# Kernel tuning notes

Hardware: AMD Instinct MI355X
Metric: run time of the kernel (lower is better)

The kernel has to match this reference:

```python
import jax, jax.numpy as jnp
import numpy as np
import math

B, N, NDIM = 8, 8192, 2
WIDTH, HEADS, OUT_C, LATENT_D = 128, 4, 128, 128
N_POINT, N_SAMPLE, RADIUS, PATCH = 128, 8, 0.2, 8
MAX_DEG = 15
POS_DIM = NDIM * (1 + 2 * MAX_DEG)  # 62
SELF_LAYERS = 3


def setup_inputs() -> dict:
    ks = jax.random.split(jax.random.key(0), 16)
    f32 = jnp.float32
    def nrm(k, shape, s=0.02):
        return jax.random.normal(k, shape, dtype=f32) * s
    W = WIDTH
    inp = {
        'points': jax.random.uniform(ks[0], (B, N, NDIM), dtype=f32),
        'pe_w': nrm(ks[1], (POS_DIM, W)), 'pe_b': jnp.zeros((W,), f32),
        'conv1_w': nrm(ks[2], (W, W + NDIM, PATCH, 1)), 'conv1_b': jnp.zeros((W,), f32),
        'conv2_w': nrm(ks[3], (W, W, PATCH, 1)), 'conv2_b': jnp.zeros((W,), f32),
        'output_tokens': jax.random.normal(ks[4], (LATENT_D, W), dtype=f32),
        'ln_pre_s': jnp.ones((W,), f32), 'ln_pre_b': jnp.zeros((W,), f32),
        'c_ln1_s': jnp.ones((W,), f32), 'c_ln1_b': jnp.zeros((W,), f32),
        'c_ln2_s': jnp.ones((W,), f32), 'c_ln2_b': jnp.zeros((W,), f32),
        'c_q_w': nrm(ks[5], (W, W)), 'c_q_b': jnp.zeros((W,), f32),
        'c_kv_w': nrm(ks[6], (W, 2 * W)), 'c_kv_b': jnp.zeros((2 * W,), f32),
        'c_proj_w': nrm(ks[7], (W, W)), 'c_proj_b': jnp.zeros((W,), f32),
        'c_ln3_s': jnp.ones((W,), f32), 'c_ln3_b': jnp.zeros((W,), f32),
        'c_mlp1_w': nrm(ks[8], (W, 4 * W)), 'c_mlp1_b': jnp.zeros((4 * W,), f32),
        'c_mlp2_w': nrm(ks[9], (4 * W, W)), 'c_mlp2_b': jnp.zeros((W,), f32),
        's_ln1_s': jnp.ones((SELF_LAYERS, W), f32), 's_ln1_b': jnp.zeros((SELF_LAYERS, W), f32),
        's_qkv_w': nrm(ks[10], (SELF_LAYERS, W, 3 * W)), 's_qkv_b': jnp.zeros((SELF_LAYERS, 3 * W), f32),
        's_proj_w': nrm(ks[11], (SELF_LAYERS, W, W)), 's_proj_b': jnp.zeros((SELF_LAYERS, W), f32),
        's_ln2_s': jnp.ones((SELF_LAYERS, W), f32), 's_ln2_b': jnp.zeros((SELF_LAYERS, W), f32),
        's_mlp1_w': nrm(ks[12], (SELF_LAYERS, W, 4 * W)), 's_mlp1_b': jnp.zeros((SELF_LAYERS, 4 * W), f32),
        's_mlp2_w': nrm(ks[13], (SELF_LAYERS, 4 * W, W)), 's_mlp2_b': jnp.zeros((SELF_LAYERS, W), f32),
        'ln_post_s': jnp.ones((W,), f32), 'ln_post_b': jnp.zeros((W,), f32),
        'out_w': nrm(ks[14], (W, OUT_C)), 'out_b': jnp.zeros((OUT_C,), f32),
    }
    return inp


def _layer_norm(x, s, b):
    m = jnp.mean(x, -1, keepdims=True)
    v = jnp.mean(jnp.square(x - m), -1, keepdims=True)
    return (x - m) * jax.lax.rsqrt(v + 1e-5) * s + b


def _posenc_nerf(x):
    # point-e nerf posenc: concat([x, sin(xb), sin(xb + pi/2)])
    scales = 2.0 ** jnp.arange(MAX_DEG, dtype=jnp.float32)
    xb = (x[..., None, :] * scales[:, None]).reshape(*x.shape[:-1], -1)
    emb = jnp.sin(jnp.concatenate([xb, xb + 0.5 * jnp.pi], axis=-1))
    return jnp.concatenate([x, emb], axis=-1)  # [..., C*(1+2*MAX_DEG)]


def _mha(q, k, v):
    b, tq, w = q.shape
    dh = w // HEADS
    qh = q.reshape(b, tq, HEADS, dh)
    kh = k.reshape(b, -1, HEADS, dh)
    vh = v.reshape(b, -1, HEADS, dh)
    scores = jnp.einsum('bqhd,bkhd->bhqk', qh, kh) * (1.0 / math.sqrt(dh))
    attn = jax.nn.softmax(scores, axis=-1)
    return jnp.einsum('bhqk,bkhd->bqhd', attn, vh).reshape(b, tq, w)


def _circ_conv(x, w, b):
    # Conv2d kernel (PATCH,1), stride 1, circular padding (PATCH//2, 0)
    p = PATCH // 2
    xp = jnp.concatenate([x[:, :, -p:], x, x[:, :, :p]], axis=2)
    y = jax.lax.conv_general_dilated(xp, w, (1, 1), 'VALID',
                                     dimension_numbers=('NCHW', 'OIHW', 'NCHW'))
    return y + b[None, :, None, None]


def _forward(points, pe_w, pe_b, conv1_w, conv1_b, conv2_w, conv2_b, output_tokens,
             ln_pre_s, ln_pre_b, c_ln1_s, c_ln1_b, c_ln2_s, c_ln2_b, c_q_w, c_q_b,
             c_kv_w, c_kv_b, c_proj_w, c_proj_b, c_ln3_s, c_ln3_b, c_mlp1_w, c_mlp1_b,
             c_mlp2_w, c_mlp2_b, s_ln1_s, s_ln1_b, s_qkv_w, s_qkv_b, s_proj_w, s_proj_b,
             s_ln2_s, s_ln2_b, s_mlp1_w, s_mlp1_b, s_mlp2_w, s_mlp2_b, ln_post_s, ln_post_b,
             out_w, out_b):
    bsz, n, _ = points.shape
    dataset_emb = _posenc_nerf(points) @ pe_w + pe_b             # [B,N,W]
    # ---- PointSetEmbedding (fps_method='first' -> first n_point centers) ----
    new_xyz = points[:, :N_POINT]                                # [B,S,2]
    sqr = jnp.sum(jnp.square(new_xyz[:, :, None] - points[:, None]), -1)  # [B,S,N]
    base = jnp.broadcast_to(jnp.arange(n, dtype=jnp.int32), sqr.shape)
    idx = jnp.where(sqr > RADIUS ** 2, n, base)
    idx = jnp.sort(idx, axis=-1)[:, :, :N_SAMPLE]
    idx = jnp.where(idx == n, idx[:, :, :1], idx)                # [B,S,K] ball-query indices
    gather = jax.vmap(lambda a, i: a[i])
    grouped_xyz = gather(points, idx) - new_xyz[:, :, None]      # [B,S,K,2] relative coords
    grouped_pts = gather(dataset_emb, idx)                       # [B,S,K,W]
    feats = jnp.concatenate([grouped_xyz, grouped_pts], -1)      # [B,S,K,W+2]
    x = jnp.transpose(feats, (0, 3, 2, 1))                       # [B,C,K,S]
    x = jax.nn.silu(_circ_conv(x, conv1_w, conv1_b))
    x = jax.nn.silu(_circ_conv(x, conv2_w, conv2_b))
    data_tokens = jnp.transpose(x.mean(axis=2), (0, 2, 1))       # [B,S,W]
    # ---- Perceiver: cross-attn then self-attn ----
    lat = jnp.broadcast_to(output_tokens[None], (bsz, LATENT_D, WIDTH))
    h = _layer_norm(jnp.concatenate([data_tokens, lat], axis=1), ln_pre_s, ln_pre_b)
    q = _layer_norm(h, c_ln1_s, c_ln1_b) @ c_q_w + c_q_b
    kv = _layer_norm(dataset_emb, c_ln2_s, c_ln2_b) @ c_kv_w + c_kv_b
    k, v = jnp.split(kv, 2, axis=-1)
    h = h + (_mha(q, k, v) @ c_proj_w + c_proj_b)
    t = _layer_norm(h, c_ln3_s, c_ln3_b)
    h = h + (jax.nn.gelu(t @ c_mlp1_w + c_mlp1_b, approximate=False) @ c_mlp2_w + c_mlp2_b)
    for i in range(SELF_LAYERS):
        qkv = _layer_norm(h, s_ln1_s[i], s_ln1_b[i]) @ s_qkv_w[i] + s_qkv_b[i]
        q, k, v = jnp.split(qkv, 3, axis=-1)
        h = h + (_mha(q, k, v) @ s_proj_w[i] + s_proj_b[i])
        t = _layer_norm(h, s_ln2_s[i], s_ln2_b[i])
        h = h + (jax.nn.gelu(t @ s_mlp1_w[i] + s_mlp1_b[i], approximate=False) @ s_mlp2_w[i] + s_mlp2_b[i])
    h = h[:, -LATENT_D:]
    return jnp.tanh(_layer_norm(h, ln_post_s, ln_post_b) @ out_w + out_b)


def reference(points, pe_w, pe_b, conv1_w, conv1_b, conv2_w, conv2_b, output_tokens,
              ln_pre_s, ln_pre_b, c_ln1_s, c_ln1_b, c_ln2_s, c_ln2_b, c_q_w, c_q_b,
              c_kv_w, c_kv_b, c_proj_w, c_proj_b, c_ln3_s, c_ln3_b, c_mlp1_w, c_mlp1_b,
              c_mlp2_w, c_mlp2_b, s_ln1_s, s_ln1_b, s_qkv_w, s_qkv_b, s_proj_w, s_proj_b,
              s_ln2_s, s_ln2_b, s_mlp1_w, s_mlp1_b, s_mlp2_w, s_mlp2_b, ln_post_s, ln_post_b,
              out_w, out_b):
    return _forward(points, pe_w, pe_b, conv1_w, conv1_b, conv2_w, conv2_b, output_tokens,
                    ln_pre_s, ln_pre_b, c_ln1_s, c_ln1_b, c_ln2_s, c_ln2_b, c_q_w, c_q_b,
                    c_kv_w, c_kv_b, c_proj_w, c_proj_b, c_ln3_s, c_ln3_b, c_mlp1_w, c_mlp1_b,
                    c_mlp2_w, c_mlp2_b, s_ln1_s, s_ln1_b, s_qkv_w, s_qkv_b, s_proj_w, s_proj_b,
                    s_ln2_s, s_ln2_b, s_mlp1_w, s_mlp1_b, s_mlp2_w, s_mlp2_b, ln_post_s, ln_post_b,
                    out_w, out_b)
```

## Files before the change

### kernel.cpp

```cpp
#include <hip/hip_runtime.h>
#include <math.h>


namespace {

constexpr int NP = 8192;
constexpr int WD = 128;
constexpr int POSD = 62;
constexpr float R2C = 0.04f;
constexpr float QSCALE = 0.17677669529663687f;
constexpr float HALFPI = 1.5707963705062866f;

typedef __bf16 bf16x8 __attribute__((ext_vector_type(8)));
typedef float f32x4 __attribute__((ext_vector_type(4)));
union U16B { uint4 u; bf16x8 h; unsigned short s[8]; };

__device__ __forceinline__ float b2f(unsigned short u) {
  unsigned v = (unsigned)u << 16;
  return __builtin_bit_cast(float, v);
}

constexpr size_t AO_WQ     = 0;
constexpr size_t AO_WKV    = 16384;
constexpr size_t AO_WPROJC = 49152;
constexpr size_t AO_WMLP1C = 65536;
constexpr size_t AO_WMLP2C = 131072;
constexpr size_t AO_WQKVS  = 196608;
constexpr size_t AO_WPROJS = 344064;
constexpr size_t AO_WMLP1S = 393216;
constexpr size_t AO_WMLP2S = 589824;
constexpr size_t AO_WOUT   = 786432;
constexpr size_t AO_W1B    = 802816;
constexpr size_t AO_W2B    = 937984;
constexpr size_t AO_TOT    = 1069056;

__global__ __launch_bounds__(256) void k_posenc(
    const float* __restrict__ pts, const float* __restrict__ pew,
    const float* __restrict__ peb, unsigned short* __restrict__ embb) {
  __shared__ float posT[62][36];
  const int tid = threadIdx.x;
  const int base = blockIdx.x * 32;
  for (int i = tid; i < 32 * POSD; i += 256) {
    int p = i / POSD, j = i % POSD;
    const float* pp = pts + (size_t)(base + p) * 2;
    float v;
    if (j < 2) {
      v = pp[j];
    } else if (j < 32) {
      int t = j - 2;
      v = sinf(pp[t & 1] * (float)(1 << (t >> 1)));
    } else {
      int t = j - 32;
      v = sinf(pp[t & 1] * (float)(1 << (t >> 1)) + HALFPI);
    }
    posT[j][p] = v;
  }
  __syncthreads();
  const int c = tid & 127, pg = tid >> 7;
  float acc[16];
  const float bias = peb[c];
#pragma unroll
  for (int k = 0; k < 16; ++k) acc[k] = bias;
  for (int j = 0; j < POSD; ++j) {
    float w = pew[j * WD + c];
    const float4 p0 = *(const float4*)&posT[j][pg * 16];
    const float4 p1 = *(const float4*)&posT[j][pg * 16 + 4];
    const float4 p2 = *(const float4*)&posT[j][pg * 16 + 8];
    const float4 p3 = *(const float4*)&posT[j][pg * 16 + 12];
    acc[0] += p0.x * w;  acc[1] += p0.y * w;
    acc[2] += p0.z * w;  acc[3] += p0.w * w;
    acc[4] += p1.x * w;  acc[5] += p1.y * w;
    acc[6] += p1.z * w;  acc[7] += p1.w * w;
    acc[8] += p2.x * w;  acc[9] += p2.y * w;
    acc[10] += p2.z * w; acc[11] += p2.w * w;
    acc[12] += p3.x * w; acc[13] += p3.y * w;
    acc[14] += p3.z * w; acc[15] += p3.w * w;
  }
#pragma unroll
  for (int k = 0; k < 16; ++k) {
    __bf16 bv = (__bf16)acc[k];
    embb[(size_t)(base + pg * 16 + k) * WD + c] = *(unsigned short*)&bv;
  }
}

__global__ __launch_bounds__(256) void k_prep(
    const float* __restrict__ wq, const float* __restrict__ wkv,
    const float* __restrict__ wprojc, const float* __restrict__ wmlp1c,
    const float* __restrict__ wmlp2c, const float* __restrict__ wqkvs,
    const float* __restrict__ wprojs, const float* __restrict__ wmlp1s,
    const float* __restrict__ wmlp2s, const float* __restrict__ wout,
    const float* __restrict__ w1, const float* __restrict__ w2,
    unsigned short* __restrict__ dst) {
  const size_t i = (size_t)blockIdx.x * 256 + threadIdx.x;
  if (i >= AO_TOT) return;
  float v;
  if (i < AO_WKV) {
    size_t j = i;            v = wq[(j & 127) * 128 + (j >> 7)];
  } else if (i < AO_WPROJC) {
    size_t j = i - AO_WKV;   v = wkv[(j & 127) * 256 + (j >> 7)];
  } else if (i < AO_WMLP1C) {
    size_t j = i - AO_WPROJC; v = wprojc[(j & 127) * 128 + (j >> 7)];
  } else if (i < AO_WMLP2C) {
    size_t j = i - AO_WMLP1C; v = wmlp1c[(j & 127) * 512 + (j >> 7)];
  } else if (i < AO_WQKVS) {
    size_t j = i - AO_WMLP2C; v = wmlp2c[(j & 511) * 128 + (j >> 9)];
  } else if (i < AO_WPROJS) {
    size_t j = i - AO_WQKVS;
    size_t L = j / 49152, jj = j % 49152;
    v = wqkvs[L * 49152 + (jj & 127) * 384 + (jj >> 7)];
  } else if (i < AO_WMLP1S) {
    size_t j = i - AO_WPROJS;
    size_t L = j / 16384, jj = j % 16384;
    v = wprojs[L * 16384 + (jj & 127) * 128 + (jj >> 7)];
  } else if (i < AO_WMLP2S) {
    size_t j = i - AO_WMLP1S;
    size_t L = j / 65536, jj = j % 65536;
    v = wmlp1s[L * 65536 + (jj & 127) * 512 + (jj >> 7)];
  } else if (i < AO_WOUT) {
    size_t j = i - AO_WMLP2S;
    size_t L = j / 65536, jj = j % 65536;
    v = wmlp2s[L * 65536 + (jj & 511) * 128 + (jj >> 9)];
  } else if (i < AO_W1B) {
    size_t j = i - AO_WOUT;  v = wout[(j & 127) * 128 + (j >> 7)];
  } else if (i < AO_W2B) {
    size_t j = i - AO_W1B;
    size_t c = j / 1056, k = j % 1056;
    v = (k < 1040) ? w1[c * 1040 + k] : 0.f;
  } else {
    size_t j = i - AO_W2B;   v = w2[(j >> 10) * 1024 + (j & 1023)];
  }
  __bf16 bv = (__bf16)v;
  dst[i] = *(unsigned short*)&bv;
}

__global__ __launch_bounds__(256) void k_kvgc(
    const unsigned short* __restrict__ embb,
    const unsigned short* __restrict__ wkvt,
    const float* __restrict__ kvbias, unsigned short* __restrict__ kb,
    unsigned short* __restrict__ vb, const float* __restrict__ lnS,
    const float* __restrict__ lnB, const float* __restrict__ pts,
    const unsigned short* __restrict__ w1b, const float* __restrict__ b1,
    const unsigned short* __restrict__ w2b, const float* __restrict__ b2,
    float* __restrict__ dtok) {
  __shared__ __align__(16) char shl[43776];
  __shared__ int sid[4][8];
  const int bx = blockIdx.x;
  const int tid = threadIdx.x;
  const int w = tid >> 6, lane = tid & 63;
  const int l15 = lane & 15, l16 = lane >> 4;

  if (bx >= 256) {
    const int kx = bx - 256;
    const size_t row0 = (size_t)kx * 32;
    unsigned short (*Ab)[136] = (unsigned short(*)[136])shl;
    unsigned short (*Bt)[136] = (unsigned short(*)[136])(shl + 8704);
    {
      const int n = tid >> 1, hf = tid & 1;
      const unsigned short* src = wkvt + ((size_t)n * 128 + hf * 64);
#pragma unroll
      for (int q8 = 0; q8 < 8; ++q8)
        *(uint4*)&Bt[n][hf * 64 + q8 * 8] = *(const uint4*)(src + q8 * 8);
    }
    {
      const int r = tid >> 3, seg = tid & 7;
      const unsigned short* ap = embb + (row0 + r) * WD + seg * 16;
      U16B w0, w1u;
      w0.u = *(const uint4*)ap;
      w1u.u = *(const uint4*)(ap + 8);
      float xv[16];
#pragma unroll
      for (int j = 0; j < 8; ++j) {
        xv[j] = b2f(w0.s[j]);
        xv[8 + j] = b2f(w1u.s[j]);
      }
      float s = 0.f, sq = 0.f;
#pragma unroll
      for (int j = 0; j < 16; ++j) { s += xv[j]; sq += xv[j] * xv[j]; }
      s += __shfl_xor(s, 1);  sq += __shfl_xor(sq, 1);
      s += __shfl_xor(s, 2);  sq += __shfl_xor(sq, 2);
      s += __shfl_xor(s, 4);  sq += __shfl_xor(sq, 4);
      const float m = s * (1.f / 128.f);
      const float var = fmaxf(sq * (1.f / 128.f) - m * m, 0.f);
      const float rinv = 1.0f / sqrtf(var + 1e-5f);
      U16B u0, u1;
#pragma unroll
      for (int j = 0; j < 16; ++j) {
        int col = seg * 16 + j;
        float y = (xv[j] - m) * rinv * lnS[col] + lnB[col];
        if (j < 8) u0.h[j] = (__bf16)y; else u1.h[j - 8] = (__bf16)y;
      }
      *(uint4*)&Ab[r][seg * 16] = u0.u;
      *(uint4*)&Ab[r][seg * 16 + 8] = u1.u;
    }
    const int rt = w >> 1, ch = w & 1;
    for (int nb = 0; nb < 2; ++nb) {
      if (nb) {
        __syncthreads();
        const int n = tid >> 1, hf = tid & 1;
        const unsigned short* src =
            wkvt + ((size_t)(128 + n) * 128 + hf * 64);
#pragma unroll
        for (int q8 = 0; q8 < 8; ++q8)
          *(uint4*)&Bt[n][hf * 64 + q8 * 8] = *(const uint4*)(src + q8 * 8);
      }
      __syncthreads();
      f32x4 acc[4];
#pragma unroll
      for (int j = 0; j < 4; ++j) acc[j] = (f32x4){0.f, 0.f, 0.f, 0.f};
#pragma unroll
      for (int kk = 0; kk < 4; ++kk) {
        U16B ua;
        ua.u = *(const uint4*)&Ab[rt * 16 + l15][kk * 32 + l16 * 8];
#pragma unroll
        for (int ct4 = 0; ct4 < 4; ++ct4) {
          U16B ub;
          ub.u =
              *(const uint4*)&Bt[(ch * 4 + ct4) * 16 + l15][kk * 32 + l16 * 8];
          acc[ct4] = __builtin_amdgcn_mfma_f32_16x16x32_bf16(ua.h, ub.h,
                                                             acc[ct4], 0, 0, 0);
        }
      }
      unsigned short* Dp = nb ? vb : kb;
#pragma unroll
      for (int ct4 = 0; ct4 < 4; ++ct4) {
        int colL = (ch * 4 + ct4) * 16 + l15;
        float bv = kvbias[nb * 128 + colL];
#pragma unroll
        for (int r = 0; r < 4; ++r) {
          size_t row = row0 + rt * 16 + l16 * 4 + r;
          __bf16 ov = (__bf16)(acc[ct4][r] + bv);
          Dp[row * 128 + colL] = *(unsigned short*)&ov;
        }
      }
    }
    return;
  }

  const int b = bx >> 5;
  const int i0 = (bx & 31) * 4;
  unsigned short* ftp  = (unsigned short*)shl;
  unsigned short* Bt1p = (unsigned short*)(shl + 8448);
  unsigned short* y1p  = (unsigned short*)shl;
  unsigned short* Bt2p = (unsigned short*)(shl + 16384);
  float* tmpp = (float*)(shl + 16384);

  {
    const int i = i0 + w;
    const float cx = pts[((size_t)b * NP + i) * 2];
    const float cy = pts[((size_t)b * NP + i) * 2 + 1];
    int cnt = 0;
    for (int j0 = 0; j0 < NP; j0 += 64) {
      int j = j0 + lane;
      float dx = pts[((size_t)b * NP + j) * 2] - cx;
      float dy = pts[((size_t)b * NP + j) * 2 + 1] - cy;
      float d2 = __fadd_rn(__fmul_rn(dx, dx), __fmul_rn(dy, dy));
      bool ok = !(d2 > R2C);
      unsigned long long m = __ballot(ok);
      int ord = cnt + __popcll(m & ((1ull << lane) - 1ull));
      if (ok && ord < 8) sid[w][ord] = j;
      cnt += (int)__popcll(m);
      if (cnt >= 8) break;
    }
    if (lane < 8 && lane >= cnt) sid[w][lane] = sid[w][0];
  }
  __syncthreads();
  {
    const int pr = tid >> 3, c16 = tid & 7;
    const int pt = pr >> 3, s = pr & 7;
    const unsigned short* src =
        embb + ((size_t)b * NP + sid[pt][s]) * WD + c16 * 16;
    U16B u0, u1;
    u0.u = *(const uint4*)src;
    u1.u = *(const uint4*)(src + 8);
#pragma unroll
    for (int j = 0; j < 8; ++j) {
      ftp[((size_t)pt * 132 + 2 + c16 * 16 + j) * 8 + s] = u0.s[j];
      ftp[((size_t)pt * 132 + 2 + c16 * 16 + 8 + j) * 8 + s] = u1.s[j];
    }
  }
  if (tid < 64) {
    int pt = tid >> 4, rem = tid & 15;
    int s = rem >> 1, d = rem & 1;
    float dv = pts[((size_t)b * NP + sid[pt][s]) * 2 + d] -
               pts[((size_t)b * NP + i0 + pt) * 2 + d];
    __bf16 bv = (__bf16)dv;
    ftp[((size_t)pt * 132 + d) * 8 + s] = *(unsigned short*)&bv;
    int pt2 = tid >> 4, cin2 = 130 + ((tid >> 3) & 1), s2 = tid & 7;
    ftp[((size_t)pt2 * 132 + cin2) * 8 + s2] = 0;
  }
  __syncthreads();
  f32x4 acc1[2][2];
#pragma unroll
  for (int t = 0; t < 2; ++t)
#pragma unroll
    for (int bt = 0; bt < 2; ++bt) acc1[t][bt] = (f32x4){0.f, 0.f, 0.f, 0.f};
  for (int ps = 0; ps < 2; ++ps) {
    const int cinbase = ps ? 68 : 0;
    const int CW = ps ? 64 : 68;
    if (ps) __syncthreads();
    {
      const int n = tid >> 3, g = tid & 7;
      const int pt = n >> 3, h = n & 7;
#pragma unroll
      for (int it = 0; it < 9; ++it) {
        int cl = g + it * 8;
        if (cl < CW) {
          int cin = cinbase + cl;
          U16B u0, u;
          u0.u = *(const uint4*)&ftp[((size_t)pt * 132 + cin) * 8];
#pragma unroll
          for (int p = 0; p < 8; ++p) u.s[p] = u0.s[(h + p + 4) & 7];
          *(uint4*)&Bt1p[n * 552 + cl * 8] = u.u;
        }
      }
    }
    __syncthreads();
    const unsigned short* w1r =
        w1b + (size_t)(w * 32 + l15) * 1056 + cinbase * 8;
    const int kit = ps ? 16 : 17;
    for (int ks = 0; ks < kit; ++ks) {
      const int k0 = ks * 32 + l16 * 8;
      U16B a0, a1, b0, b1u;
      a0.u = *(const uint4*)(w1r + k0);
      a1.u = *(const uint4*)(w1r + 16 * 1056 + k0);
      b0.u = *(const uint4*)&Bt1p[l15 * 552 + k0];
      b1u.u = *(const uint4*)&Bt1p[(16 + l15) * 552 + k0];
      acc1[0][0] = __builtin_amdgcn_mfma_f32_16x16x32_bf16(a0.h, b0.h,
                                                           acc1[0][0], 0, 0, 0);
      acc1[0][1] = __builtin_amdgcn_mfma_f32_16x16x32_bf16(a0.h, b1u.h,
                                                           acc1[0][1], 0, 0, 0);
      acc1[1][0] = __builtin_amdgcn_mfma_f32_16x16x32_bf16(a1.h, b0.h,
                                                           acc1[1][0], 0, 0, 0);
      acc1[1][1] = __builtin_amdgcn_mfma_f32_16x16x32_bf16(a1.h, b1u.h,
                                                           acc1[1][1], 0, 0, 0);
    }
  }
  __syncthreads();
  {
#pragma unroll
    for (int t = 0; t < 2; ++t)
#pragma unroll
      for (int bt = 0; bt < 2; ++bt) {
        const int n = bt * 16 + l15;
        const int pt = n >> 3, h = n & 7;
#pragma unroll
        for (int r = 0; r < 4; ++r) {
          int c = w * 32 + t * 16 + l16 * 4 + r;
          float x = acc1[t][bt][r] + b1[c];
          float sy = x / (1.f + __expf(-x));
          __bf16 bh = (__bf16)sy;
          unsigned short bits = *(unsigned short*)&bh;
          size_t yb = ((size_t)pt * 128 + c) * 16;
          y1p[yb + h] = bits;
          if (h == 0) y1p[yb + 8] = bits;
        }
      }
  }
  f32x4 acc2[2][3];
#pragma unroll
  for (int t = 0; t < 2; ++t)
#pragma unroll
    for (int bt = 0; bt < 3; ++bt) acc2[t][bt] = (f32x4){0.f, 0.f, 0.f, 0.f};
  for (int ps = 0; ps < 4; ++ps) {
    __syncthreads();
    {
      const int g = tid & 7;
      for (int n2 = tid >> 3; n2 < 38; n2 += 32) {
        const int pt = n2 / 9, h2 = n2 % 9;
#pragma unroll
        for (int it = 0; it < 4; ++it) {
          int cl = g + it * 8;
          U16B o;
          if (n2 < 36) {
            int c1 = ps * 32 + cl;
            size_t yb = ((size_t)pt * 128 + c1) * 16;
            U16B u0;
            u0.u = *(const uint4*)&y1p[yb];
            unsigned short yv[9];
#pragma unroll
            for (int j = 0; j < 8; ++j) yv[j] = u0.s[j];
            yv[8] = y1p[yb + 8];
#pragma unroll
            for (int p = 0; p < 8; ++p) o.s[p] = yv[(h2 + p + 5) % 9];
          } else {
            o.u.x = o.u.y = o.u.z = o.u.w = 0;
          }
          *(uint4*)&Bt2p[n2 * 264 + cl * 8] = o.u;
        }
      }
    }
    __syncthreads();
    const unsigned short* w2r =
        w2b + (size_t)(w * 32 + l15) * 1024 + ps * 256;
    int r2 = 32 + l15;
    if (r2 > 37) r2 = 37;
#pragma unroll
    for (int ks = 0; ks < 8; ++ks) {
      const int k0 = ks * 32 + l16 * 8;
      U16B a0, a1, b0, b1u, b2u;
      a0.u = *(const uint4*)(w2r + k0);
      a1.u = *(const uint4*)(w2r + 16 * 1024 + k0);
      b0.u = *(const uint4*)&Bt2p[l15 * 264 + k0];
      b1u.u = *(const uint4*)&Bt2p[(16 + l15) * 264 + k0];
      b2u.u = *(const uint4*)&Bt2p[r2 * 264 + k0];
      acc2[0][0] = __builtin_amdgcn_mfma_f32_16x16x32_bf16(a0.h, b0.h,
                                                           acc2[0][0], 0, 0, 0);
      acc2[0][1] = __builtin_amdgcn_mfma_f32_16x16x32_bf16(a0.h, b1u.h,
                                                           acc2[0][1], 0, 0, 0);
      acc2[0][2] = __builtin_amdgcn_mfma_f32_16x16x32_bf16(a0.h, b2u.h,
                                                           acc2[0][2], 0, 0, 0);
      acc2[1][0] = __builtin_amdgcn_mfma_f32_16x16x32_bf16(a1.h, b0.h,
                                                           acc2[1][0], 0, 0, 0);
      acc2[1][1] = __builtin_amdgcn_mfma_f32_16x16x32_bf16(a1.h, b1u.h,
                                                           acc2[1][1], 0, 0, 0);
      acc2[1][2] = __builtin_amdgcn_mfma_f32_16x16x32_bf16(a1.h, b2u.h,
                                                           acc2[1][2], 0, 0, 0);
    }
  }
  __syncthreads();
  {
#pragma unroll
    for (int t = 0; t < 2; ++t)
#pragma unroll
      for (int bt = 0; bt < 3; ++bt) {
        const int n2 = bt * 16 + l15;
        if (n2 < 36) {
          const int h2 = n2 % 9;
          const float wgt = (h2 == 0) ? 2.f : 1.f;
#pragma unroll
          for (int r = 0; r < 4; ++r) {
            int c = w * 32 + t * 16 + l16 * 4 + r;
            float x = acc2[t][bt][r] + b2[c];
            tmpp[n2 * 132 + c] = wgt * (x / (1.f + __expf(-x)));
          }
        }
      }
  }
  __syncthreads();
#pragma unroll
  for (int k = 0; k < 2; ++k) {
    int idx = tid + k * 256;
    int pt = idx >> 7, c = idx & 127;
    float ssum = 0.f;
#pragma unroll
    for (int h2 = 0; h2 < 9; ++h2) ssum += tmpp[(pt * 9 + h2) * 132 + c];
    dtok[((size_t)b * 128 + i0 + pt) * WD + c] = ssum / 10.0f;
  }
}

__global__ __launch_bounds__(64) void k_concat_ln(
    const float* __restrict__ dtok, const float* __restrict__ otok,
    const float* __restrict__ g, const float* __restrict__ bta,
    float* __restrict__ h0) {
  const int row = blockIdx.x;
  const int b = row >> 8, t = row & 255;
  const int lane = threadIdx.x;
  const float* src = (t < 128) ? (dtok + ((size_t)b * 128 + t) * WD)
                               : (otok + (size_t)(t - 128) * WD);
  const float2 x2 = *(const float2*)(src + lane * 2);
  float s = x2.x + x2.y;
  float sq = x2.x * x2.x + x2.y * x2.y;
#pragma unroll
  for (int o = 1; o < 64; o <<= 1) {
    s += __shfl_xor(s, o);
    sq += __shfl_xor(sq, o);
  }
  float m = s * (1.f / 128.f);
  float var = fmaxf(sq * (1.f / 128.f) - m * m, 0.f);
  float r = 1.0f / sqrtf(var + 1e-5f);
  int c = lane * 2;
  float2 o2;
  o2.x = (x2.x - m) * r * g[c] + bta[c];
  o2.y = (x2.y - m) * r * g[c + 1] + bta[c + 1];
  *(float2*)(h0 + (size_t)row * WD + c) = o2;
}

template <int ABF, int OBF, int COMB>
__global__ __launch_bounds__(256) void k_bgemm16(
    const void* __restrict__ A, int lda, const unsigned short* __restrict__ wt,
    const float* __restrict__ bias, const float* __restrict__ res, int ldres,
    void* __restrict__ D, int ldd, int K, int act,
    const float* __restrict__ lnS, const float* __restrict__ lnB, int keep,
    int skip, float oscale, int scaleCols,
    const unsigned short* __restrict__ opart, const float* __restrict__ lbuf,
    int S) {
  __shared__ unsigned short Ab[16][136];
  __shared__ unsigned short Bt[64][136];
  const int tid = threadIdx.x;
  const int row0 = blockIdx.x * 16;
  const int col0 = blockIdx.y * 64;
  const int w = tid >> 6, lane = tid & 63;
  const int l15 = lane & 15, l16 = lane >> 4;
  f32x4 acc = (f32x4){0.f, 0.f, 0.f, 0.f};
  for (int kt = 0; kt < K; kt += 128) {
    if (kt) __syncthreads();
    {
      const int n = tid >> 2, q = tid & 3;
      const unsigned short* src = wt + (size_t)(col0 + n) * K + kt + q * 32;
      *(uint4*)&Bt[n][q * 32] = *(const uint4*)src;
      *(uint4*)&Bt[n][q * 32 + 8] = *(const uint4*)(src + 8);
// ... 25 lines not shown
        const int srow = (grow / keep) * (keep + skip) + skip + grow % keep;
        const unsigned short* ap =
            (const unsigned short*)A + (size_t)srow * lda + kt + seg * 8;
        *(uint4*)&Ab[r][seg * 8] = *(const uint4*)ap;
      } else {
        const int srow = (grow / keep) * (keep + skip) + skip + grow % keep;
        const float* ap = (const float*)A + (size_t)srow * lda + kt + seg * 8;
        float4 v0 = *(const float4*)ap;
        float4 v1 = *(const float4*)(ap + 4);
        float xv[8] = {v0.x, v0.y, v0.z, v0.w, v1.x, v1.y, v1.z, v1.w};
        if (lnS != nullptr) {
          float s = 0.f, sq = 0.f;
#pragma unroll
          for (int j = 0; j < 8; ++j) { s += xv[j]; sq += xv[j] * xv[j]; }
          s += __shfl_xor(s, 1);  sq += __shfl_xor(sq, 1);
          s += __shfl_xor(s, 2);  sq += __shfl_xor(sq, 2);
          s += __shfl_xor(s, 4);  sq += __shfl_xor(sq, 4);
          s += __shfl_xor(s, 8);  sq += __shfl_xor(sq, 8);
          const float m = s * (1.f / 128.f);
          const float var = fmaxf(sq * (1.f / 128.f) - m * m, 0.f);
          const float rinv = 1.0f / sqrtf(var + 1e-5f);
#pragma unroll
          for (int j = 0; j < 8; ++j) {
            int col = seg * 8 + j;
            xv[j] = (xv[j] - m) * rinv * lnS[col] + lnB[col];
          }
        }
        U16B u0;
#pragma unroll
        for (int j = 0; j < 8; ++j) u0.h[j] = (__bf16)xv[j];
        *(uint4*)&Ab[r][seg * 8] = u0.u;
      }
    }
    __syncthreads();
#pragma unroll
    for (int kk = 0; kk < 4; ++kk) {
      U16B ua, ub;
      ua.u = *(const uint4*)&Ab[l15][kk * 32 + l16 * 8];
      ub.u = *(const uint4*)&Bt[w * 16 + l15][kk * 32 + l16 * 8];
      acc = __builtin_amdgcn_mfma_f32_16x16x32_bf16(ua.h, ub.h, acc, 0, 0, 0);
    }
  }
  {
    const int colL = w * 16 + l15;
    const int col = col0 + colL;
    const float bv = bias[col];
#pragma unroll
    for (int r = 0; r < 4; ++r) {
      const int row = row0 + l16 * 4 + r;
      float x = acc[r] + bv;
      if (col0 < scaleCols) x *= oscale;
      if (act == 1) x = 0.5f * x * (1.0f + erff(x * 0.7071067811865476f));
      else if (act == 2) x = tanhf(x);
      if (res != nullptr) x += res[(size_t)row * ldres + col];
      if (OBF) {
        __bf16 ov = (__bf16)x;
        ((unsigned short*)D)[(size_t)row * ldd + col] = *(unsigned short*)&ov;
      } else {
        ((float*)D)[(size_t)row * ldd + col] = x;
      }
    }
  }
}

__global__ __launch_bounds__(256) void k_attn_mfma(
    const unsigned short* __restrict__ Q, int qs,
    const unsigned short* __restrict__ K, int ks,
    const unsigned short* __restrict__ V, int vs,
    unsigned short* __restrict__ opart, float* __restrict__ lbuf, int Tk,
    int S, int CH) {
  const int bx = blockIdx.x;
  const int s = bx % S;
  const int bh = bx / S;
  const int h = bh & 3, b = bh >> 2;
  const int tid = threadIdx.x;
  const int w = tid >> 6, lane = tid & 63;
  const int l15 = lane & 15, l16 = lane >> 4;

  __shared__ unsigned short Vt[32 * 68];
  __shared__ unsigned short Pl[4][16 * 72];

  bf16x8 qf[4];
#pragma unroll
  for (int m = 0; m < 4; ++m) {
    U16B u;
    u.u = *(const uint4*)(Q + (size_t)(b * 256 + w * 64 + m * 16 + l15) * qs +
                          h * 32 + l16 * 8);
    qf[m] = u.h;
  }
  U16B uones;
#pragma unroll
  for (int j = 0; j < 8; ++j) uones.h[j] = (__bf16)1.0f;
  const bf16x8 ones = uones.h;

  f32x4 o[4][2];
#pragma unroll
  for (int m = 0; m < 4; ++m)
#pragma unroll
    for (int d = 0; d < 2; ++d) o[m][d] = (f32x4){0.f, 0.f, 0.f, 0.f};
  f32x4 lsum[4];
#pragma unroll
  for (int m = 0; m < 4; ++m) lsum[m] = (f32x4){0.f, 0.f, 0.f, 0.f};

  const int kt0 = s * CH;
  for (int kt = kt0; kt < kt0 + CH; kt += 64) {
    __syncthreads();
// ... 94 lines not shown
  const float* conv1_b  = (const float*)d_in[4];
  const float* conv2_w  = (const float*)d_in[5];
  const float* conv2_b  = (const float*)d_in[6];
  const float* otok     = (const float*)d_in[7];
  const float* ln_pre_s = (const float*)d_in[8];
  const float* ln_pre_b = (const float*)d_in[9];
  const float* c_ln1_s  = (const float*)d_in[10];
  const float* c_ln1_b  = (const float*)d_in[11];
  const float* c_ln2_s  = (const float*)d_in[12];
  const float* c_ln2_b  = (const float*)d_in[13];
  const float* c_q_w    = (const float*)d_in[14];
  const float* c_q_b    = (const float*)d_in[15];
  const float* c_kv_w   = (const float*)d_in[16];
  const float* c_kv_b   = (const float*)d_in[17];
  const float* c_proj_w = (const float*)d_in[18];
  const float* c_proj_b = (const float*)d_in[19];
  const float* c_ln3_s  = (const float*)d_in[20];
  const float* c_ln3_b  = (const float*)d_in[21];
  const float* c_mlp1_w = (const float*)d_in[22];
  const float* c_mlp1_b = (const float*)d_in[23];
  const float* c_mlp2_w = (const float*)d_in[24];
  const float* c_mlp2_b = (const float*)d_in[25];
  const float* s_ln1_s  = (const float*)d_in[26];
  const float* s_ln1_b  = (const float*)d_in[27];
  const float* s_qkv_w  = (const float*)d_in[28];
  const float* s_qkv_b  = (const float*)d_in[29];
  const float* s_proj_w = (const float*)d_in[30];
  const float* s_proj_b = (const float*)d_in[31];
  const float* s_ln2_s  = (const float*)d_in[32];
  const float* s_ln2_b  = (const float*)d_in[33];
  const float* s_mlp1_w = (const float*)d_in[34];
  const float* s_mlp1_b = (const float*)d_in[35];
  const float* s_mlp2_w = (const float*)d_in[36];
  const float* s_mlp2_b = (const float*)d_in[37];
  const float* lnpost_s = (const float*)d_in[38];
  const float* lnpost_b = (const float*)d_in[39];
  const float* out_w    = (const float*)d_in[40];
  const float* out_b    = (const float*)d_in[41];

  char* ws = (char*)d_ws;
  constexpr size_t MB = 1024 * 1024;
  unsigned short* embb = (unsigned short*)(ws);
  unsigned short* kbuf = (unsigned short*)(ws + 32 * MB);
  unsigned short* vbuf = (unsigned short*)(ws + 48 * MB);
  char*  b3   = ws + 64 * MB;
  float* dtok = (float*)(b3);
  float* hbuf = (float*)(b3 + 524288);
  unsigned short* qbuf = (unsigned short*)(b3 + 524288 + 1048576);
  unsigned short* mid = (unsigned short*)(b3 + 524288 + 3145728);
  unsigned short* qkv = (unsigned short*)(b3 + 524288 + 7340032);
  unsigned short* arena = (unsigned short*)(b3 + 524288 + 10485760);
  unsigned short* opart = (unsigned short*)(ws);
  float* lbuf  = (float*)(b3 + 16 * MB);

  const int IDK = 1 << 28;

  k_prep<<<(int)((AO_TOT + 255) / 256), 256, 0, stream>>>(
      c_q_w, c_kv_w, c_proj_w, c_mlp1_w, c_mlp2_w, s_qkv_w, s_proj_w,
      s_mlp1_w, s_mlp2_w, out_w, conv1_w, conv2_w, arena);
  k_posenc<<<2048, 256, 0, stream>>>(pts, pe_w, pe_b, embb);
  k_kvgc<<<2304, 256, 0, stream>>>(embb, arena + AO_WKV, c_kv_b, kbuf, vbuf,
                                   c_ln2_s, c_ln2_b, pts, arena + AO_W1B,
                                   conv1_b, arena + AO_W2B, conv2_b, dtok);
  k_concat_ln<<<2048, 64, 0, stream>>>(dtok, otok, ln_pre_s, ln_pre_b, hbuf);
  k_bgemm16<0, 1, 0><<<dim3(128, 2), 256, 0, stream>>>(
      hbuf, 128, arena + AO_WQ, c_q_b, nullptr, 0, qbuf, 128, 128, 0, c_ln1_s,
      c_ln1_b, IDK, 0, QSCALE, 128, nullptr, nullptr, 0);
  k_attn_mfma<<<1024, 256, 0, stream>>>(qbuf, 128, kbuf, 128, vbuf, 128,
                                        opart, lbuf, 8192, 32, 256);
  k_bgemm16<0, 0, 1><<<dim3(128, 2), 256, 0, stream>>>(
      nullptr, 128, arena + AO_WPROJC, c_proj_b, hbuf, 128, hbuf, 128, 128, 0,
      nullptr, nullptr, IDK, 0, 1.f, 0, opart, lbuf, 32);
  k_bgemm16<0, 1, 0><<<dim3(128, 8), 256, 0, stream>>>(
      hbuf, 128, arena + AO_WMLP1C, c_mlp1_b, nullptr, 0, mid, 512, 128, 1,
      c_ln3_s, c_ln3_b, IDK, 0, 1.f, 0, nullptr, nullptr, 0);
  k_bgemm16<1, 0, 0><<<dim3(128, 2), 256, 0, stream>>>(
      mid, 512, arena + AO_WMLP2C, c_mlp2_b, hbuf, 128, hbuf, 128, 512, 0,
      nullptr, nullptr, IDK, 0, 1.f, 0, nullptr, nullptr, 0);
  for (int i = 0; i < 3; ++i) {
    k_bgemm16<0, 1, 0><<<dim3(128, 6), 256, 0, stream>>>(
        hbuf, 128, arena + AO_WQKVS + (size_t)i * 49152, s_qkv_b + i * 384,
        nullptr, 0, qkv, 384, 128, 0, s_ln1_s + i * 128, s_ln1_b + i * 128,
        IDK, 0, QSCALE, 128, nullptr, nullptr, 0);
    k_attn_mfma<<<128, 256, 0, stream>>>(qkv, 384, qkv + 128, 384, qkv + 256,
                                         384, opart, lbuf, 256, 4, 64);
    k_bgemm16<0, 0, 1><<<dim3(128, 2), 256, 0, stream>>>(
        nullptr, 128, arena + AO_WPROJS + (size_t)i * 16384,
        s_proj_b + i * 128, hbuf, 128, hbuf, 128, 128, 0, nullptr, nullptr,
        IDK, 0, 1.f, 0, opart, lbuf, 4);
    k_bgemm16<0, 1, 0><<<dim3(128, 8), 256, 0, stream>>>(
        hbuf, 128, arena + AO_WMLP1S + (size_t)i * 65536, s_mlp1_b + i * 512,
        nullptr, 0, mid, 512, 128, 1, s_ln2_s + i * 128, s_ln2_b + i * 128,
        IDK, 0, 1.f, 0, nullptr, nullptr, 0);
    k_bgemm16<1, 0, 0><<<dim3(128, 2), 256, 0, stream>>>(
        mid, 512, arena + AO_WMLP2S + (size_t)i * 65536, s_mlp2_b + i * 128,
        hbuf, 128, hbuf, 128, 512, 0, nullptr, nullptr, IDK, 0, 1.f, 0,
        nullptr, nullptr, 0);
  }
  k_bgemm16<0, 0, 0><<<dim3(64, 2), 256, 0, stream>>>(
      hbuf, 128, arena + AO_WOUT, out_b, nullptr, 0, (float*)d_out, 128, 128,
      2, lnpost_s, lnpost_b, 128, 128, 1.f, 0, nullptr, nullptr, 0);
}
```

Baseline: 231.6 us.

## Split fused grouping-conv kernel into im2col plus generic GEMM launches

The monolithic k_kvgc kernel, which did ball-query grouping, two patch convolutions and the KV projection in one launch, is split into separate kernels. The new path is a ball-query/im2col kernel, a generic bgemm with a SiLU epilogue for conv1, a second im2col, a bgemm for conv2, a mean-reduction kernel, and a standalone LN+KV kernel. The aim is better parallelism and occupancy for the conv GEMMs, which previously ran in only 256 blocks with large shared memory. In exchange it adds several launches and global-memory round trips for the im2col buffers and intermediate activations.

```diff
diff --git a/kernel.cpp b/kernel.cpp
--- a/kernel.cpp
+++ b/kernel.cpp
@@ -31,8 +31,8 @@
 constexpr size_t AO_WMLP2S = 589824;
 constexpr size_t AO_WOUT   = 786432;
 constexpr size_t AO_W1B    = 802816;
-constexpr size_t AO_W2B    = 937984;
-constexpr size_t AO_TOT    = 1069056;
+constexpr size_t AO_W2B    = 950272;
+constexpr size_t AO_TOT    = 1081344;
 
 __global__ __launch_bounds__(256) void k_posenc(
     const float* __restrict__ pts, const float* __restrict__ pew,
@@ -124,7 +124,7 @@
     size_t j = i - AO_WOUT;  v = wout[(j & 127) * 128 + (j >> 7)];
   } else if (i < AO_W2B) {
     size_t j = i - AO_W1B;
-    size_t c = j / 1056, k = j % 1056;
+    size_t c = j / 1152, k = j % 1152;
     v = (k < 1040) ? w1[c * 1040 + k] : 0.f;
   } else {
     size_t j = i - AO_W2B;   v = w2[(j >> 10) * 1024 + (j & 1023)];
@@ -133,319 +133,193 @@
   dst[i] = *(unsigned short*)&bv;
 }
 
-__global__ __launch_bounds__(256) void k_kvgc(
+__global__ __launch_bounds__(256) void k_kvln(
     const unsigned short* __restrict__ embb,
     const unsigned short* __restrict__ wkvt,
     const float* __restrict__ kvbias, unsigned short* __restrict__ kb,
     unsigned short* __restrict__ vb, const float* __restrict__ lnS,
-    const float* __restrict__ lnB, const float* __restrict__ pts,
-    const unsigned short* __restrict__ w1b, const float* __restrict__ b1,
-    const unsigned short* __restrict__ w2b, const float* __restrict__ b2,
-    float* __restrict__ dtok) {
-  __shared__ __align__(16) char shl[43776];
-  __shared__ int sid[4][8];
-  const int bx = blockIdx.x;
+    const float* __restrict__ lnB) {
+  __shared__ unsigned short Ab[32][136];
+  __shared__ unsigned short Bt[128][136];
   const int tid = threadIdx.x;
   const int w = tid >> 6, lane = tid & 63;
   const int l15 = lane & 15, l16 = lane >> 4;
-
-  if (bx >= 256) {
-    const int kx = bx - 256;
-    const size_t row0 = (size_t)kx * 32;
-    unsigned short (*Ab)[136] = (unsigned short(*)[136])shl;
-    unsigned short (*Bt)[136] = (unsigned short(*)[136])(shl + 8704);
-    {
+  const size_t row0 = (size_t)blockIdx.x * 32;
+  {
+    const int n = tid >> 1, hf = tid & 1;
+    const unsigned short* src = wkvt + ((size_t)n * 128 + hf * 64);
+#pragma unroll
+    for (int q8 = 0; q8 < 8; ++q8)
+      *(uint4*)&Bt[n][hf * 64 + q8 * 8] = *(const uint4*)(src + q8 * 8);
+  }
+  {
+    const int r = tid >> 3, seg = tid & 7;
+    const unsigned short* ap = embb + (row0 + r) * WD + seg * 16;
+    U16B w0, w1u;
+    w0.u = *(const uint4*)ap;
+    w1u.u = *(const uint4*)(ap + 8);
+    float xv[16];
+#pragma unroll
+    for (int j = 0; j < 8; ++j) {
+      xv[j] = b2f(w0.s[j]);
+      xv[8 + j] = b2f(w1u.s[j]);
+    }
+    float s = 0.f, sq = 0.f;
+#pragma unroll
+    for (int j = 0; j < 16; ++j) { s += xv[j]; sq += xv[j] * xv[j]; }
+    s += __shfl_xor(s, 1);  sq += __shfl_xor(sq, 1);
+    s += __shfl_xor(s, 2);  sq += __shfl_xor(sq, 2);
+    s += __shfl_xor(s, 4);  sq += __shfl_xor(sq, 4);
+    const float m = s * (1.f / 128.f);
+    const float var = fmaxf(sq * (1.f / 128.f) - m * m, 0.f);
+    const float rinv = 1.0f / sqrtf(var + 1e-5f);
+    U16B u0, u1;
+#pragma unroll
+    for (int j = 0; j < 16; ++j) {
+      int col = seg * 16 + j;
+      float y = (xv[j] - m) * rinv * lnS[col] + lnB[col];
+      if (j < 8) u0.h[j] = (__bf16)y; else u1.h[j - 8] = (__bf16)y;
+    }
+    *(uint4*)&Ab[r][seg * 16] = u0.u;
+    *(uint4*)&Ab[r][seg * 16 + 8] = u1.u;
+  }
+  const int rt = w >> 1, ch = w & 1;
+  for (int nb = 0; nb < 2; ++nb) {
+    if (nb) {
+      __syncthreads();
       const int n = tid >> 1, hf = tid & 1;
-      const unsigned short* src = wkvt + ((size_t)n * 128 + hf * 64);
+      const unsigned short* src = wkvt + ((size_t)(128 + n) * 128 + hf * 64);
 #pragma unroll
       for (int q8 = 0; q8 < 8; ++q8)
         *(uint4*)&Bt[n][hf * 64 + q8 * 8] = *(const uint4*)(src + q8 * 8);
     }
-    {
-      const int r = tid >> 3, seg = tid & 7;
-      const unsigned short* ap = embb + (row0 + r) * WD + seg * 16;
-      U16B w0, w1u;
-      w0.u = *(const uint4*)ap;
-      w1u.u = *(const uint4*)(ap + 8);
-      float xv[16];
-#pragma unroll
-      for (int j = 0; j < 8; ++j) {
-        xv[j] = b2f(w0.s[j]);
-        xv[8 + j] = b2f(w1u.s[j]);
+    __syncthreads();
+    f32x4 acc[4];
+#pragma unroll
+    for (int j = 0; j < 4; ++j) acc[j] = (f32x4){0.f, 0.f, 0.f, 0.f};
+#pragma unroll
+    for (int kk = 0; kk < 4; ++kk) {
+      U16B ua;
+      ua.u = *(const uint4*)&Ab[rt * 16 + l15][kk * 32 + l16 * 8];
+#pragma unroll
+      for (int ct4 = 0; ct4 < 4; ++ct4) {
+        U16B ub;
+        ub.u = *(const uint4*)&Bt[(ch * 4 + ct4) * 16 + l15][kk * 32 + l16 * 8];
+        acc[ct4] = __builtin_amdgcn_mfma_f32_16x16x32_bf16(ua.h, ub.h,
+                                                           acc[ct4], 0, 0, 0);
       }
-      float s = 0.f, sq = 0.f;
-#pragma unroll
-      for (int j = 0; j < 16; ++j) { s += xv[j]; sq += xv[j] * xv[j]; }
-      s += __shfl_xor(s, 1);  sq += __shfl_xor(sq, 1);
-      s += __shfl_xor(s, 2);  sq += __shfl_xor(sq, 2);
-      s += __shfl_xor(s, 4);  sq += __shfl_xor(sq, 4);
-      const float m = s * (1.f / 128.f);
-      const float var = fmaxf(sq * (1.f / 128.f) - m * m, 0.f);
-      const float rinv = 1.0f / sqrtf(var + 1e-5f);
-      U16B u0, u1;
-#pragma unroll
-      for (int j = 0; j < 16; ++j) {
-        int col = seg * 16 + j;
-        float y = (xv[j] - m) * rinv * lnS[col] + lnB[col];
-        if (j < 8) u0.h[j] = (__bf16)y; else u1.h[j - 8] = (__bf16)y;
+    }
+    unsigned short* Dp = nb ? vb : kb;
+#pragma unroll
+    for (int ct4 = 0; ct4 < 4; ++ct4) {
+      int colL = (ch * 4 + ct4) * 16 + l15;
+      float bv = kvbias[nb * 128 + colL];
+#pragma unroll
+      for (int r = 0; r < 4; ++r) {
+        size_t row = row0 + rt * 16 + l16 * 4 + r;
+        __bf16 ov = (__bf16)(acc[ct4][r] + bv);
+        Dp[row * 128 + colL] = *(unsigned short*)&ov;
       }
-      *(uint4*)&Ab[r][seg * 16] = u0.u;
-      *(uint4*)&Ab[r][seg * 16 + 8] = u1.u;
-    }
-    const int rt = w >> 1, ch = w & 1;
-    for (int nb = 0; nb < 2; ++nb) {
-      if (nb) {
-        __syncthreads();
-        const int n = tid >> 1, hf = tid & 1;
-        const unsigned short* src =
-            wkvt + ((size_t)(128 + n) * 128 + hf * 64);
-#pragma unroll
-        for (int q8 = 0; q8 < 8; ++q8)
-          *(uint4*)&Bt[n][hf * 64 + q8 * 8] = *(const uint4*)(src + q8 * 8);
-      }
-      __syncthreads();
-      f32x4 acc[4];
-#pragma unroll
-      for (int j = 0; j < 4; ++j) acc[j] = (f32x4){0.f, 0.f, 0.f, 0.f};
-#pragma unroll
-      for (int kk = 0; kk < 4; ++kk) {
-        U16B ua;
-        ua.u = *(const uint4*)&Ab[rt * 16 + l15][kk * 32 + l16 * 8];
-#pragma unroll
-        for (int ct4 = 0; ct4 < 4; ++ct4) {
-          U16B ub;
-          ub.u =
-              *(const uint4*)&Bt[(ch * 4 + ct4) * 16 + l15][kk * 32 + l16 * 8];
-          acc[ct4] = __builtin_amdgcn_mfma_f32_16x16x32_bf16(ua.h, ub.h,
-                                                             acc[ct4], 0, 0, 0);
-        }
-      }
-      unsigned short* Dp = nb ? vb : kb;
-#pragma unroll
-      for (int ct4 = 0; ct4 < 4; ++ct4) {
-        int colL = (ch * 4 + ct4) * 16 + l15;
-        float bv = kvbias[nb * 128 + colL];
-#pragma unroll
-        for (int r = 0; r < 4; ++r) {
-          size_t row = row0 + rt * 16 + l16 * 4 + r;
-          __bf16 ov = (__bf16)(acc[ct4][r] + bv);
-          Dp[row * 128 + colL] = *(unsigned short*)&ov;
-        }
-      }
-    }
-    return;
-  }
-
-  const int b = bx >> 5;
-  const int i0 = (bx & 31) * 4;
-  unsigned short* ftp  = (unsigned short*)shl;
-  unsigned short* Bt1p = (unsigned short*)(shl + 8448);
-  unsigned short* y1p  = (unsigned short*)shl;
-  unsigned short* Bt2p = (unsigned short*)(shl + 16384);
-  float* tmpp = (float*)(shl + 16384);
-
-  {
-    const int i = i0 + w;
-    const float cx = pts[((size_t)b * NP + i) * 2];
-    const float cy = pts[((size_t)b * NP + i) * 2 + 1];
-    int cnt = 0;
-    for (int j0 = 0; j0 < NP; j0 += 64) {
-      int j = j0 + lane;
-      float dx = pts[((size_t)b * NP + j) * 2] - cx;
-      float dy = pts[((size_t)b * NP + j) * 2 + 1] - cy;
-      float d2 = __fadd_rn(__fmul_rn(dx, dx), __fmul_rn(dy, dy));
-      bool ok = !(d2 > R2C);
-      unsigned long long m = __ballot(ok);
-      int ord = cnt + __popcll(m & ((1ull << lane) - 1ull));
-      if (ok && ord < 8) sid[w][ord] = j;
-      cnt += (int)__popcll(m);
-      if (cnt >= 8) break;
-    }
-    if (lane < 8 && lane >= cnt) sid[w][lane] = sid[w][0];
-  }
+    }
+  }
+}
+
+__global__ __launch_bounds__(256) void k_im2col1(
+    const float* __restrict__ pts, const unsigned short* __restrict__ embb,
+    unsigned short* __restrict__ B1g) {
+  __shared__ unsigned short ft[132][8];
+  __shared__ int sid[8];
+  __shared__ int wcnt[4];
+  const int bx = blockIdx.x;
+  const int b = bx >> 7, i = bx & 127;
+  const int tid = threadIdx.x;
+  const int w = tid >> 6, lane = tid & 63;
+  const float cx = pts[((size_t)b * NP + i) * 2];
+  const float cy = pts[((size_t)b * NP + i) * 2 + 1];
+  int cnt = 0;
+  for (int j0 = 0; j0 < NP; j0 += 256) {
+    const int j = j0 + tid;
+    float dx = pts[((size_t)b * NP + j) * 2] - cx;
+    float dy = pts[((size_t)b * NP + j) * 2 + 1] - cy;
+    float d2 = __fadd_rn(__fmul_rn(dx, dx), __fmul_rn(dy, dy));
+    bool ok = !(d2 > R2C);
+    unsigned long long m = __ballot(ok);
+    if (lane == 0) wcnt[w] = (int)__popcll(m);
+    __syncthreads();
+    int pre = cnt, tot = cnt;
+#pragma unroll
+    for (int ww = 0; ww < 4; ++ww) {
+      int c4 = wcnt[ww];
+      if (ww < w) pre += c4;
+      tot += c4;
+    }
+    if (ok) {
+      int ord = pre + (int)__popcll(m & ((1ull << lane) - 1ull));
+      if (ord < 8) sid[ord] = j;
+    }
+    __syncthreads();
+    cnt = tot;
+    if (cnt >= 8) break;
+  }
+  if (tid >= cnt && tid < 8) sid[tid] = sid[0];
   __syncthreads();
   {
-    const int pr = tid >> 3, c16 = tid & 7;
-    const int pt = pr >> 3, s = pr & 7;
-    const unsigned short* src =
-        embb + ((size_t)b * NP + sid[pt][s]) * WD + c16 * 16;
-    U16B u0, u1;
-    u0.u = *(const uint4*)src;
-    u1.u = *(const uint4*)(src + 8);
-#pragma unroll
-    for (int j = 0; j < 8; ++j) {
-      ftp[((size_t)pt * 132 + 2 + c16 * 16 + j) * 8 + s] = u0.s[j];
-      ftp[((size_t)pt * 132 + 2 + c16 * 16 + 8 + j) * 8 + s] = u1.s[j];
-    }
-  }
-  if (tid < 64) {
-    int pt = tid >> 4, rem = tid & 15;
-    int s = rem >> 1, d = rem & 1;
-    float dv = pts[((size_t)b * NP + sid[pt][s]) * 2 + d] -
-               pts[((size_t)b * NP + i0 + pt) * 2 + d];
+    const int s = tid >> 5, c4 = tid & 31;
+    uint2 u = *(const uint2*)(embb + ((size_t)b * NP + sid[s]) * WD + c4 * 4);
+    const unsigned short* us = (const unsigned short*)&u;
+#pragma unroll
+    for (int j2 = 0; j2 < 4; ++j2) ft[2 + c4 * 4 + j2][s] = us[j2];
+  }
+  if (tid < 16) {
+    int s = tid >> 1, d = tid & 1;
+    float dv = pts[((size_t)b * NP + sid[s]) * 2 + d] -
+               pts[((size_t)b * NP + i) * 2 + d];
     __bf16 bv = (__bf16)dv;
-    ftp[((size_t)pt * 132 + d) * 8 + s] = *(unsigned short*)&bv;
-    int pt2 = tid >> 4, cin2 = 130 + ((tid >> 3) & 1), s2 = tid & 7;
-    ftp[((size_t)pt2 * 132 + cin2) * 8 + s2] = 0;
+    ft[d][s] = *(unsigned short*)&bv;
+  } else if (tid < 32) {
+    int idx = tid - 16;
+    ft[130 + (idx >> 3)][idx & 7] = 0;
   }
   __syncthreads();
-  f32x4 acc1[2][2];
-#pragma unroll
-  for (int t = 0; t < 2; ++t)
-#pragma unroll
-    for (int bt = 0; bt < 2; ++bt) acc1[t][bt] = (f32x4){0.f, 0.f, 0.f, 0.f};
-  for (int ps = 0; ps < 2; ++ps) {
-    const int cinbase = ps ? 68 : 0;
-    const int CW = ps ? 64 : 68;
-    if (ps) __syncthreads();
-    {
-      const int n = tid >> 3, g = tid & 7;
-      const int pt = n >> 3, h = n & 7;
-#pragma unroll
-      for (int it = 0; it < 9; ++it) {
-        int cl = g + it * 8;
-        if (cl < CW) {
-          int cin = cinbase + cl;
-          U16B u0, u;
-          u0.u = *(const uint4*)&ftp[((size_t)pt * 132 + cin) * 8];
-#pragma unroll
-          for (int p = 0; p < 8; ++p) u.s[p] = u0.s[(h + p + 4) & 7];
-          *(uint4*)&Bt1p[n * 552 + cl * 8] = u.u;
-        }
+  for (int h = 0; h < 8; ++h) {
+    if (tid < 144) {
+      U16B u;
+      if (tid < 132) {
+        U16B f;
+        f.u = *(const uint4*)&ft[tid][0];
+#pragma unroll
+        for (int p = 0; p < 8; ++p) u.s[p] = f.s[(h + p + 4) & 7];
+      } else {
+        u.u.x = u.u.y = u.u.z = u.u.w = 0;
       }
-    }
-    __syncthreads();
-    const unsigned short* w1r =
-        w1b + (size_t)(w * 32 + l15) * 1056 + cinbase * 8;
-    const int kit = ps ? 16 : 17;
-    for (int ks = 0; ks < kit; ++ks) {
-      const int k0 = ks * 32 + l16 * 8;
-      U16B a0, a1, b0, b1u;
-      a0.u = *(const uint4*)(w1r + k0);
-      a1.u = *(const uint4*)(w1r + 16 * 1056 + k0);
-      b0.u = *(const uint4*)&Bt1p[l15 * 552 + k0];
-      b1u.u = *(const uint4*)&Bt1p[(16 + l15) * 552 + k0];
-      acc1[0][0] = __builtin_amdgcn_mfma_f32_16x16x32_bf16(a0.h, b0.h,
-                                                           acc1[0][0], 0, 0, 0);
-      acc1[0][1] = __builtin_amdgcn_mfma_f32_16x16x32_bf16(a0.h, b1u.h,
-                                                           acc1[0][1], 0, 0, 0);
-      acc1[1][0] = __builtin_amdgcn_mfma_f32_16x16x32_bf16(a1.h, b0.h,
-                                                           acc1[1][0], 0, 0, 0);
-      acc1[1][1] = __builtin_amdgcn_mfma_f32_16x16x32_bf16(a1.h, b1u.h,
-                                                           acc1[1][1], 0, 0, 0);
-    }
-  }
-  __syncthreads();
-  {
-#pragma unroll
-    for (int t = 0; t < 2; ++t)
-#pragma unroll
-      for (int bt = 0; bt < 2; ++bt) {
-        const int n = bt * 16 + l15;
-        const int pt = n >> 3, h = n & 7;
-#pragma unroll
-        for (int r = 0; r < 4; ++r) {
-          int c = w * 32 + t * 16 + l16 * 4 + r;
-          float x = acc1[t][bt][r] + b1[c];
-          float sy = x / (1.f + __expf(-x));
-          __bf16 bh = (__bf16)sy;
-          unsigned short bits = *(unsigned short*)&bh;
-          size_t yb = ((size_t)pt * 128 + c) * 16;
-          y1p[yb + h] = bits;
-          if (h == 0) y1p[yb + 8] = bits;
-        }
-      }
-  }
-  f32x4 acc2[2][3];
-#pragma unroll
-  for (int t = 0; t < 2; ++t)
-#pragma unroll
-    for (int bt = 0; bt < 3; ++bt) acc2[t][bt] = (f32x4){0.f, 0.f, 0.f, 0.f};
-  for (int ps = 0; ps < 4; ++ps) {
-    __syncthreads();
-    {
-      const int g = tid & 7;
-      for (int n2 = tid >> 3; n2 < 38; n2 += 32) {
-        const int pt = n2 / 9, h2 = n2 % 9;
-#pragma unroll
-        for (int it = 0; it < 4; ++it) {
-          int cl = g + it * 8;
-          U16B o;
-          if (n2 < 36) {
-            int c1 = ps * 32 + cl;
-            size_t yb = ((size_t)pt * 128 + c1) * 16;
-            U16B u0;
-            u0.u = *(const uint4*)&y1p[yb];
-            unsigned short yv[9];
-#pragma unroll
-            for (int j = 0; j < 8; ++j) yv[j] = u0.s[j];
-            yv[8] = y1p[yb + 8];
-#pragma unroll
-            for (int p = 0; p < 8; ++p) o.s[p] = yv[(h2 + p + 5) % 9];
-          } else {
-            o.u.x = o.u.y = o.u.z = o.u.w = 0;
-          }
-          *(uint4*)&Bt2p[n2 * 264 + cl * 8] = o.u;
-        }
-      }
-    }
-    __syncthreads();
-    const unsigned short* w2r =
-        w2b + (size_t)(w * 32 + l15) * 1024 + ps * 256;
-    int r2 = 32 + l15;
-    if (r2 > 37) r2 = 37;
-#pragma unroll
-    for (int ks = 0; ks < 8; ++ks) {
-      const int k0 = ks * 32 + l16 * 8;
-      U16B a0, a1, b0, b1u, b2u;
-      a0.u = *(const uint4*)(w2r + k0);
-      a1.u = *(const uint4*)(w2r + 16 * 1024 + k0);
-      b0.u = *(const uint4*)&Bt2p[l15 * 264 + k0];
-      b1u.u = *(const uint4*)&Bt2p[(16 + l15) * 264 + k0];
-      b2u.u = *(const uint4*)&Bt2p[r2 * 264 + k0];
-      acc2[0][0] = __builtin_amdgcn_mfma_f32_16x16x32_bf16(a0.h, b0.h,
-                                                           acc2[0][0], 0, 0, 0);
-      acc2[0][1] = __builtin_amdgcn_mfma_f32_16x16x32_bf16(a0.h, b1u.h,
-                                                           acc2[0][1], 0, 0, 0);
-      acc2[0][2] = __builtin_amdgcn_mfma_f32_16x16x32_bf16(a0.h, b2u.h,
-                                                           acc2[0][2], 0, 0, 0);
-      acc2[1][0] = __builtin_amdgcn_mfma_f32_16x16x32_bf16(a1.h, b0.h,
-                                                           acc2[1][0], 0, 0, 0);
-      acc2[1][1] = __builtin_amdgcn_mfma_f32_16x16x32_bf16(a1.h, b1u.h,
-                                                           acc2[1][1], 0, 0, 0);
-      acc2[1][2] = __builtin_amdgcn_mfma_f32_16x16x32_bf16(a1.h, b2u.h,
-                                                           acc2[1][2], 0, 0, 0);
-    }
-  }
-  __syncthreads();
-  {
-#pragma unroll
-    for (int t = 0; t < 2; ++t)
-#pragma unroll
-      for (int bt = 0; bt < 3; ++bt) {
-        const int n2 = bt * 16 + l15;
-        if (n2 < 36) {
-          const int h2 = n2 % 9;
-          const float wgt = (h2 == 0) ? 2.f : 1.f;
-#pragma unroll
-          for (int r = 0; r < 4; ++r) {
-            int c = w * 32 + t * 16 + l16 * 4 + r;
-            float x = acc2[t][bt][r] + b2[c];
-            tmpp[n2 * 132 + c] = wgt * (x / (1.f + __expf(-x)));
-          }
-        }
-      }
-  }
-  __syncthreads();
-#pragma unroll
-  for (int k = 0; k < 2; ++k) {
-    int idx = tid + k * 256;
-    int pt = idx >> 7, c = idx & 127;
-    float ssum = 0.f;
-#pragma unroll
-    for (int h2 = 0; h2 < 9; ++h2) ssum += tmpp[(pt * 9 + h2) * 132 + c];
-    dtok[((size_t)b * 128 + i0 + pt) * WD + c] = ssum / 10.0f;
-  }
+      *(uint4*)&B1g[((size_t)bx * 8 + h) * 1152 + tid * 8] = u.u;
+    }
+  }
+}
+
+__global__ __launch_bounds__(128) void k_im2col2(
+    const unsigned short* __restrict__ y1g, unsigned short* __restrict__ B2g) {
+  const int bx = blockIdx.x;
+  const int pt = bx / 9, h2 = bx % 9;
+  const int c1 = threadIdx.x;
+  U16B u;
+#pragma unroll
+  for (int p = 0; p < 8; ++p) {
+    int hs = (h2 + p + 5) % 9;
+    if (hs == 8) hs = 0;
+    u.s[p] = y1g[((size_t)pt * 8 + hs) * 128 + c1];
+  }
+  *(uint4*)&B2g[(size_t)bx * 1024 + c1 * 8] = u.u;
+}
+
+__global__ __launch_bounds__(256) void k_redmean(
+    const float* __restrict__ y2g, float* __restrict__ dtok) {
+  const int idx = blockIdx.x * 256 + threadIdx.x;
+  const int pt = idx >> 7, c = idx & 127;
+  float s = y2g[((size_t)pt * 9) * 128 + c];
+#pragma unroll
+  for (int h2 = 0; h2 < 9; ++h2) s += y2g[((size_t)pt * 9 + h2) * 128 + c];
+  dtok[(size_t)idx] = s / 10.0f;
 }
 
 __global__ __launch_bounds__(64) void k_concat_ln(
@@ -577,6 +451,7 @@
       if (col0 < scaleCols) x *= oscale;
       if (act == 1) x = 0.5f * x * (1.0f + erff(x * 0.7071067811865476f));
       else if (act == 2) x = tanhf(x);
+      else if (act == 3) x = x / (1.f + __expf(-x));
       if (res != nullptr) x += res[(size_t)row * ldres + col];
       if (OBF) {
         __bf16 ov = (__bf16)x;
@@ -777,6 +652,10 @@
   unsigned short* arena = (unsigned short*)(b3 + 524288 + 10485760);
   unsigned short* opart = (unsigned short*)(ws);
   float* lbuf  = (float*)(b3 + 16 * MB);
+  unsigned short* B1g = (unsigned short*)(ws + 16 * MB);
+  unsigned short* B2g = B1g;
+  unsigned short* y1g = (unsigned short*)(ws + 35 * MB);
+  float* y2g = (float*)(ws + 38 * MB);
 
   const int IDK = 1 << 28;
 
@@ -784,9 +663,17 @@
       c_q_w, c_kv_w, c_proj_w, c_mlp1_w, c_mlp2_w, s_qkv_w, s_proj_w,
       s_mlp1_w, s_mlp2_w, out_w, conv1_w, conv2_w, arena);
   k_posenc<<<2048, 256, 0, stream>>>(pts, pe_w, pe_b, embb);
-  k_kvgc<<<2304, 256, 0, stream>>>(embb, arena + AO_WKV, c_kv_b, kbuf, vbuf,
-                                   c_ln2_s, c_ln2_b, pts, arena + AO_W1B,
-                                   conv1_b, arena + AO_W2B, conv2_b, dtok);
+  k_im2col1<<<1024, 256, 0, stream>>>(pts, embb, B1g);
+  k_bgemm16<1, 1, 0><<<dim3(512, 2), 256, 0, stream>>>(
+      B1g, 1152, arena + AO_W1B, conv1_b, nullptr, 0, y1g, 128, 1152, 3,
+      nullptr, nullptr, IDK, 0, 1.f, 0, nullptr, nullptr, 0);
+  k_im2col2<<<9216, 128, 0, stream>>>(y1g, B2g);
+  k_bgemm16<1, 0, 0><<<dim3(576, 2), 256, 0, stream>>>(
+      B2g, 1024, arena + AO_W2B, conv2_b, nullptr, 0, y2g, 128, 1024, 3,
+      nullptr, nullptr, IDK, 0, 1.f, 0, nullptr, nullptr, 0);
+  k_redmean<<<512, 256, 0, stream>>>(y2g, dtok);
+  k_kvln<<<2048, 256, 0, stream>>>(embb, arena + AO_WKV, c_kv_b, kbuf, vbuf,
+                                   c_ln2_s, c_ln2_b);
   k_concat_ln<<<2048, 64, 0, stream>>>(dtok, otok, ln_pre_s, ln_pre_b, hbuf);
   k_bgemm16<0, 1, 0><<<dim3(128, 2), 256, 0, stream>>>(
       hbuf, 128, arena + AO_WQ, c_q_b, nullptr, 0, qbuf, 128, 128, 0, c_ln1_s,
```

Measured after the change: 248.8 us. 1.07x slower.
